# Kernel optimization log

Hardware: AMD Instinct MI355X
Metric: run time of the kernel (lower is better)

The kernel has to match this reference:

```python
import jax, jax.numpy as jnp
import numpy as np

L, B, D, N_LAYERS = 2048, 32, 1024, 4


def setup_inputs() -> dict:
    key = jax.random.key(0)
    ks = jax.random.split(key, 5)
    # PyTorch Linear default init: U(-1/sqrt(fan_in), 1/sqrt(fan_in))
    bound = 1.0 / np.sqrt(D)
    x = jax.random.normal(ks[0], (L, B, D), dtype=jnp.float32)
    A_log = jnp.log(0.99) * jnp.ones((D,), dtype=jnp.float32)  # matches torch init
    layers_W = jax.random.uniform(ks[1], (N_LAYERS, D, D), jnp.float32, -bound, bound)
    layers_b = jax.random.uniform(ks[2], (N_LAYERS, D), jnp.float32, -bound, bound)
    head_W = jax.random.uniform(ks[3], (1, D), jnp.float32, -bound, bound)
    head_b = jax.random.uniform(ks[4], (1,), jnp.float32, -bound, bound)
    return {"x": x, "A_log": A_log, "layers_W": layers_W, "layers_b": layers_b,
            "head_W": head_W, "head_b": head_b}


def reference(x, A_log, layers_W, layers_b, head_W, head_b):
    Lx, Bx, Dx = x.shape
    # log_P[t] = (t+1) * A_log  (cumsum of the constant log_A along time)
    log_P = jnp.cumsum(jnp.broadcast_to(A_log[None, None, :], (Lx, Bx, Dx)), axis=0)
    P = jnp.exp(log_P)                       # [L, B, D]
    h = P * jnp.cumsum(x / P, axis=0)        # diagonal linear SSM scan
    for i in range(layers_W.shape[0]):
        h = jnp.tanh(jnp.einsum('lbd,ed->lbe', h, layers_W[i]) + layers_b[i])
    out = jnp.einsum('lbd,ed->lbe', h, head_W) + head_b  # [L, B, 1]
    return out.squeeze(-1)                   # [L, B]
```

## Files before the change

kernel.cpp:

```cpp
#include <hip/hip_runtime.h>
#include <cstdint>
#include <cstddef>

#define LSEQ 2048
#define BB   32
#define DD   1024
#define NLAYERS 4
#define MM   (LSEQ*BB)
#define BD   (BB*DD)
#define CHUNK 32
#define NCHUNK (LSEQ/CHUNK)

typedef _Float16 f16;
typedef __attribute__((ext_vector_type(8))) _Float16 f16x8;
typedef __attribute__((ext_vector_type(4))) float f32x4;


__global__ void scan_pass1(const float* __restrict__ x, const float* __restrict__ Alog,
                           f16* __restrict__ h, float* __restrict__ carry) {
    int tid = blockIdx.x * blockDim.x + threadIdx.x;
    int bd  = tid & (BD - 1);
    int c   = tid >> 15;
    float a = expf(Alog[bd & (DD - 1)]);
    size_t base = (size_t)c * CHUNK * BD + bd;
    float hv = 0.f;
#pragma unroll
    for (int i = 0; i < CHUNK; ++i) {
        hv = a * hv + x[base + (size_t)i * BD];
        h[base + (size_t)i * BD] = (f16)hv;
    }
    carry[c * BD + bd] = hv;
}

__global__ void scan_pass2(const float* __restrict__ Alog, float* __restrict__ carry) {
    int bd = blockIdx.x * blockDim.x + threadIdx.x;
    float d32 = expf((float)CHUNK * Alog[bd & (DD - 1)]);
    float cin = 0.f;
    for (int c = 0; c < NCHUNK; ++c) {
        float co = carry[c * BD + bd];
        carry[c * BD + bd] = cin;
        cin = d32 * cin + co;
    }
}

__global__ void scan_pass3(const float* __restrict__ Alog, const float* __restrict__ carry,
                           f16* __restrict__ h) {
    int tid = blockIdx.x * blockDim.x + threadIdx.x;
    int bd  = tid & (BD - 1);
    int c   = tid >> 15;
    float a   = expf(Alog[bd & (DD - 1)]);
    float cin = carry[c * BD + bd];
    size_t base = (size_t)c * CHUNK * BD + bd;
    float p = a;
#pragma unroll
    for (int i = 0; i < CHUNK; ++i) {
        size_t idx = base + (size_t)i * BD;
        float hv = (float)h[idx] + p * cin;
        h[idx] = (f16)hv;
        p *= a;
    }
}


__global__ void cvt_w(const float* __restrict__ w, f16* __restrict__ o, int n) {
    int i = (blockIdx.x * blockDim.x + threadIdx.x) * 4;
    if (i + 3 < n) {
        float4 v = *(const float4*)&w[i];
        o[i + 0] = (f16)v.x; o[i + 1] = (f16)v.y;
        o[i + 2] = (f16)v.z; o[i + 3] = (f16)v.w;
    }
}


#define BM 256
#define BN 256
#define BK 64
#define KK 1024
#define NN 1024
#define NKTILE (KK / BK)

__device__ __forceinline__ void gload_lds16(const void* g, void* l) {
    __builtin_amdgcn_global_load_lds((const __attribute__((address_space(1))) unsigned int*)g,
                                     (__attribute__((address_space(3))) unsigned int*)l,
                                     16, 0, 0);
}

__device__ __forceinline__ void stage_half(const f16* __restrict__ gbase, f16* region, int tid) {
#pragma unroll
    for (int j = 0; j < 2; ++j) {
        int s = tid + j * 512;
        int r = s >> 3;
        int c = (s & 7) ^ (r & 7);
        gload_lds16(gbase + (size_t)r * KK + c * 8, region + (size_t)s * 8);
    }
}

__device__ __forceinline__ void stage_tile(const f16* __restrict__ gA, const f16* __restrict__ gW,
                                           f16* As, f16* Bs, int tid) {
    stage_half(gA,                    As,        tid);
    stage_half(gA + (size_t)128 * KK, As + 8192, tid);
    stage_half(gW,                    Bs,        tid);
    stage_half(gW + (size_t)128 * KK, Bs + 8192, tid);
}

__device__ __forceinline__ f16x8 rd(const f16* base, int row, int chunk) {
    int c = chunk ^ (row & 7);
    return *(const f16x8*)(base + row * 64 + c * 8);
}

__device__ __forceinline__ void read12(const f16* Abase, const f16* Bbase,
                                       int arow, int brow, int kc,
                                       f16x8 a[8], f16x8 b[4]) {
#pragma unroll
    for (int m = 0; m < 8; ++m) a[m] = rd(Abase, arow + m * 16, kc);
#pragma unroll
    for (int n = 0; n < 4; ++n) b[n] = rd(Bbase, brow + n * 16, kc);
}

__device__ __forceinline__ float tanh_fast(float z) {
    float e = __expf(2.f * z);
    return 1.f - 2.f / (e + 1.f);
}

#define BAR() do { __builtin_amdgcn_sched_barrier(0); __builtin_amdgcn_s_barrier(); \
                   __builtin_amdgcn_sched_barrier(0); } while (0)

#define MFMA32(av, bv) do {                                                     \
    __builtin_amdgcn_s_setprio(1);                                              \
    _Pragma("unroll")                                                           \
    for (int m = 0; m < 8; ++m)                                                 \
        _Pragma("unroll")                                                       \
        for (int n = 0; n < 4; ++n)                                             \
            acc[m][n] = __builtin_amdgcn_mfma_f32_16x16x32_f16(av[m], bv[n],    \
                                                               acc[m][n], 0, 0, 0); \
    __builtin_amdgcn_s_setprio(0);                                              \
} while (0)

__global__ __launch_bounds__(512, 2) void gemm_tanh(const f16* __restrict__ A,
                                                    const f16* __restrict__ W,
                                                    const float* __restrict__ bias,
                                                    f16* __restrict__ C) {
    __shared__ f16 As[2][BM * BK];
    __shared__ f16 Bs[2][BN * BK];

    const int tid  = threadIdx.x;
    const int lane = tid & 63;
    const int wid  = tid >> 6;
    const int wr   = wid >> 2;
    const int wc   = wid & 3;

    const int cpx = gridDim.x >> 3;
    const int lin = ((int)blockIdx.x & 7) * cpx + ((int)blockIdx.x >> 3);
    const int tm  = (lin >> 2) * BM;
    const int tn  = (lin & 3) * BN;

    const f16* Ab = A + (size_t)tm * KK;
    const f16* Wb = W + (size_t)tn * KK;

    const int fr = lane & 15;
    const int fc = lane >> 4;

    f32x4 acc[8][4];
#pragma unroll
    for (int i = 0; i < 8; ++i)
#pragma unroll
        for (int j = 0; j < 4; ++j)
            acc[i][j] = (f32x4){0.f, 0.f, 0.f, 0.f};

    stage_tile(Ab,      Wb,      &As[0][0], &Bs[0][0], tid);
    stage_tile(Ab + 64, Wb + 64, &As[1][0], &Bs[1][0], tid);
    asm volatile("s_waitcnt vmcnt(8)" ::: "memory");
    BAR();

    const int arow = wr * 128 + fr;
    const int brow = wc * 64  + fr;

    for (int it = 0; it < NKTILE / 2; ++it) {
        const bool pf = (it + 1 < NKTILE / 2);
        f16x8 a0[8], b0[4], a1[8], b1[4];

        read12(&As[0][0], &Bs[0][0], arow, brow, fc,     a0, b0);
        read12(&As[0][0], &Bs[0][0], arow, brow, 4 + fc, a1, b1);
        MFMA32(a0, b0);
        asm volatile("s_waitcnt lgkmcnt(0)" ::: "memory");
        BAR();
        if (pf) stage_tile(Ab + (size_t)(2 * it + 2) * BK, Wb + (size_t)(2 * it + 2) * BK,
                           &As[0][0], &Bs[0][0], tid);
        MFMA32(a1, b1);
        if (pf) asm volatile("s_waitcnt vmcnt(8)" ::: "memory");
        else    asm volatile("s_waitcnt vmcnt(0)" ::: "memory");
        BAR();

        read12(&As[1][0], &Bs[1][0], arow, brow, fc,     a0, b0);
        read12(&As[1][0], &Bs[1][0], arow, brow, 4 + fc, a1, b1);
        MFMA32(a0, b0);
        asm volatile("s_waitcnt lgkmcnt(0)" ::: "memory");
        BAR();
        if (pf) stage_tile(Ab + (size_t)(2 * it + 3) * BK, Wb + (size_t)(2 * it + 3) * BK,
                           &As[1][0], &Bs[1][0], tid);
        MFMA32(a1, b1);
        if (pf) asm volatile("s_waitcnt vmcnt(8)" ::: "memory");
        BAR();
    }

#pragma unroll
    for (int mi = 0; mi < 8; ++mi) {
        const int r0 = tm + wr * 128 + mi * 16 + (fc << 2);
#pragma unroll
        for (int ni = 0; ni < 4; ++ni) {
            const int c = tn + wc * 64 + ni * 16 + fr;
            const float bv = bias[c];
#pragma unroll
            for (int q = 0; q < 4; ++q) {
                float z = acc[mi][ni][q] + bv;
                C[(size_t)(r0 + q) * NN + c] = (f16)tanh_fast(z);
            }
        }
    }
}


__global__ void head_k(const f16* __restrict__ h, const float* __restrict__ hw,
                       const float* __restrict__ hb, float* __restrict__ out) {
    const int row  = blockIdx.x * 4 + (threadIdx.x >> 6);
    const int lane = threadIdx.x & 63;
    const f16* hr = h + (size_t)row * DD;
    float s = 0.f;
#pragma unroll
    for (int j = 0; j < DD / 64; ++j) {
        int d = lane + j * 64;
        s += (float)hr[d] * hw[d];
    }
#pragma unroll
    for (int o = 32; o > 0; o >>= 1) s += __shfl_down(s, o, 64);
    if (lane == 0) out[row] = s + hb[0];
}


extern "C" void kernel_launch(void* const* d_in, const int* in_sizes, int n_in,
                              void* d_out, int out_size, void* d_ws, size_t ws_size,
                              hipStream_t stream) {
    const float* x    = (const float*)d_in[0];
    const float* Alog = (const float*)d_in[1];
    const float* Wls  = (const float*)d_in[2];
    const float* bls  = (const float*)d_in[3];
    const float* hw   = (const float*)d_in[4];
    const float* hb   = (const float*)d_in[5];
    float* out = (float*)d_out;

    char* ws = (char*)d_ws;
    const size_t hbytes = (size_t)MM * DD * sizeof(f16);
    f16* h0 = (f16*)ws;
    f16* h1 = (f16*)(ws + hbytes);
    char* scratch = ws + 2 * hbytes;
    float* carry = (float*)scratch;
    f16*   wf    = (f16*)scratch;

    scan_pass1<<<(NCHUNK * BD) / 256, 256, 0, stream>>>(x, Alog, h0, carry);
    scan_pass2<<<BD / 256, 256, 0, stream>>>(Alog, carry);
    scan_pass3<<<(NCHUNK * BD) / 256, 256, 0, stream>>>(Alog, carry, h0);

    cvt_w<<<(NLAYERS * DD * DD / 4) / 256, 256, 0, stream>>>(Wls, wf, NLAYERS * DD * DD);

    dim3 grid((MM / BM) * (NN / BN)), blk(512);
    gemm_tanh<<<grid, blk, 0, stream>>>(h0, wf + 0 * (DD * DD), bls + 0 * DD, h1);
    gemm_tanh<<<grid, blk, 0, stream>>>(h1, wf + 1 * (DD * DD), bls + 1 * DD, h0);
    gemm_tanh<<<grid, blk, 0, stream>>>(h0, wf + 2 * (DD * DD), bls + 2 * DD, h1);
    gemm_tanh<<<grid, blk, 0, stream>>>(h1, wf + 3 * (DD * DD), bls + 3 * DD, h0);

    head_k<<<MM / 4, 256, 0, stream>>>(h0, hw, hb, out);
}
```

Baseline: 762.7 us.

## Switch GEMM to BK=32 with triple-buffered LDS and one barrier per k-tile

Replaces the double-buffered BK=64 main loop, which used two half-tile MFMA phases and two barriers per tile, with a BK=32 triple-buffered pipeline. Each iteration issues the global->LDS load for tile t+2, reads tile t from LDS, runs one MFMA block, waits on vmcnt and then does a single barrier. The LDS swizzle is reworked for 32-element rows. The aim is to keep more loads in flight and cut barrier overhead per MFMA. In exchange the tiles are smaller, so there are twice as many iterations and barriers overall, with less MFMA work between syncs. LDS use drops from 128KB to 96KB.

New measurement: 837.3 us. 9.8% more time.

```diff
diff --git a/kernel.cpp b/kernel.cpp
--- a/kernel.cpp
+++ b/kernel.cpp
@@ -74,10 +74,10 @@
 
 #define BM 256
 #define BN 256
-#define BK 64
+#define BK 32
 #define KK 1024
 #define NN 1024
-#define NKTILE (KK / BK)
+#define NKT (KK / BK)
 
 __device__ __forceinline__ void gload_lds16(const void* g, void* l) {
     __builtin_amdgcn_global_load_lds((const __attribute__((address_space(1))) unsigned int*)g,
@@ -85,36 +85,27 @@
                                      16, 0, 0);
 }
 
-__device__ __forceinline__ void stage_half(const f16* __restrict__ gbase, f16* region, int tid) {
+__device__ __forceinline__ void stage_kt(const f16* __restrict__ gA, const f16* __restrict__ gW,
+                                         f16* As_, f16* Bs_, int tid) {
 #pragma unroll
     for (int j = 0; j < 2; ++j) {
         int s = tid + j * 512;
-        int r = s >> 3;
-        int c = (s & 7) ^ (r & 7);
-        gload_lds16(gbase + (size_t)r * KK + c * 8, region + (size_t)s * 8);
-    }
-}
-
-__device__ __forceinline__ void stage_tile(const f16* __restrict__ gA, const f16* __restrict__ gW,
-                                           f16* As, f16* Bs, int tid) {
-    stage_half(gA,                    As,        tid);
-    stage_half(gA + (size_t)128 * KK, As + 8192, tid);
-    stage_half(gW,                    Bs,        tid);
-    stage_half(gW + (size_t)128 * KK, Bs + 8192, tid);
+        int r = s >> 2;
+        int c = (s & 3) ^ ((r >> 1) & 3);
+        gload_lds16(gA + (size_t)r * KK + c * 8, As_ + (size_t)s * 8);
+    }
+#pragma unroll
+    for (int j = 0; j < 2; ++j) {
+        int s = tid + j * 512;
+        int r = s >> 2;
+        int c = (s & 3) ^ ((r >> 1) & 3);
+        gload_lds16(gW + (size_t)r * KK + c * 8, Bs_ + (size_t)s * 8);
+    }
 }
 
 __device__ __forceinline__ f16x8 rd(const f16* base, int row, int chunk) {
-    int c = chunk ^ (row & 7);
-    return *(const f16x8*)(base + row * 64 + c * 8);
-}
-
-__device__ __forceinline__ void read12(const f16* Abase, const f16* Bbase,
-                                       int arow, int brow, int kc,
-                                       f16x8 a[8], f16x8 b[4]) {
-#pragma unroll
-    for (int m = 0; m < 8; ++m) a[m] = rd(Abase, arow + m * 16, kc);
-#pragma unroll
-    for (int n = 0; n < 4; ++n) b[n] = rd(Bbase, brow + n * 16, kc);
+    int c = chunk ^ ((row >> 1) & 3);
+    return *(const f16x8*)(base + row * 32 + c * 8);
 }
 
 __device__ __forceinline__ float tanh_fast(float z) {
@@ -124,24 +115,13 @@
 
 #define BAR() do { __builtin_amdgcn_sched_barrier(0); __builtin_amdgcn_s_barrier(); \
                    __builtin_amdgcn_sched_barrier(0); } while (0)
-
-#define MFMA32(av, bv) do {                                                     \
-    __builtin_amdgcn_s_setprio(1);                                              \
-    _Pragma("unroll")                                                           \
-    for (int m = 0; m < 8; ++m)                                                 \
-        _Pragma("unroll")                                                       \
-        for (int n = 0; n < 4; ++n)                                             \
-            acc[m][n] = __builtin_amdgcn_mfma_f32_16x16x32_f16(av[m], bv[n],    \
-                                                               acc[m][n], 0, 0, 0); \
-    __builtin_amdgcn_s_setprio(0);                                              \
-} while (0)
 
 __global__ __launch_bounds__(512, 2) void gemm_tanh(const f16* __restrict__ A,
                                                     const f16* __restrict__ W,
                                                     const float* __restrict__ bias,
                                                     f16* __restrict__ C) {
-    __shared__ f16 As[2][BM * BK];
-    __shared__ f16 Bs[2][BN * BK];
+    __shared__ f16 As[3][BM * BK];
+    __shared__ f16 Bs[3][BN * BK];
 
     const int tid  = threadIdx.x;
     const int lane = tid & 63;
@@ -167,40 +147,39 @@
         for (int j = 0; j < 4; ++j)
             acc[i][j] = (f32x4){0.f, 0.f, 0.f, 0.f};
 
-    stage_tile(Ab,      Wb,      &As[0][0], &Bs[0][0], tid);
-    stage_tile(Ab + 64, Wb + 64, &As[1][0], &Bs[1][0], tid);
-    asm volatile("s_waitcnt vmcnt(8)" ::: "memory");
+    stage_kt(Ab,      Wb,      &As[0][0], &Bs[0][0], tid);
+    stage_kt(Ab + BK, Wb + BK, &As[1][0], &Bs[1][0], tid);
+    asm volatile("s_waitcnt vmcnt(4)" ::: "memory");
     BAR();
 
     const int arow = wr * 128 + fr;
     const int brow = wc * 64  + fr;
 
-    for (int it = 0; it < NKTILE / 2; ++it) {
-        const bool pf = (it + 1 < NKTILE / 2);
-        f16x8 a0[8], b0[4], a1[8], b1[4];
-
-        read12(&As[0][0], &Bs[0][0], arow, brow, fc,     a0, b0);
-        read12(&As[0][0], &Bs[0][0], arow, brow, 4 + fc, a1, b1);
-        MFMA32(a0, b0);
-        asm volatile("s_waitcnt lgkmcnt(0)" ::: "memory");
-        BAR();
-        if (pf) stage_tile(Ab + (size_t)(2 * it + 2) * BK, Wb + (size_t)(2 * it + 2) * BK,
-                           &As[0][0], &Bs[0][0], tid);
-        MFMA32(a1, b1);
-        if (pf) asm volatile("s_waitcnt vmcnt(8)" ::: "memory");
-        else    asm volatile("s_waitcnt vmcnt(0)" ::: "memory");
-        BAR();
-
-        read12(&As[1][0], &Bs[1][0], arow, brow, fc,     a0, b0);
-        read12(&As[1][0], &Bs[1][0], arow, brow, 4 + fc, a1, b1);
-        MFMA32(a0, b0);
-        asm volatile("s_waitcnt lgkmcnt(0)" ::: "memory");
-        BAR();
-        if (pf) stage_tile(Ab + (size_t)(2 * it + 3) * BK, Wb + (size_t)(2 * it + 3) * BK,
-                           &As[1][0], &Bs[1][0], tid);
-        MFMA32(a1, b1);
-        if (pf) asm volatile("s_waitcnt vmcnt(8)" ::: "memory");
-        BAR();
+#pragma unroll
+    for (int t = 0; t < NKT; ++t) {
+        const f16* Ac = &As[t % 3][0];
+        const f16* Bc = &Bs[t % 3][0];
+
+        if (t + 2 < NKT)
+            stage_kt(Ab + (size_t)(t + 2) * BK, Wb + (size_t)(t + 2) * BK,
+                     &As[(t + 2) % 3][0], &Bs[(t + 2) % 3][0], tid);
+
+        f16x8 a[8], b[4];
+#pragma unroll
+        for (int m = 0; m < 8; ++m) a[m] = rd(Ac, arow + m * 16, fc);
+#pragma unroll
+        for (int n = 0; n < 4; ++n) b[n] = rd(Bc, brow + n * 16, fc);
+        __builtin_amdgcn_s_setprio(1);
+#pragma unroll
+        for (int m = 0; m < 8; ++m)
+#pragma unroll
+            for (int n = 0; n < 4; ++n)
+                acc[m][n] = __builtin_amdgcn_mfma_f32_16x16x32_f16(a[m], b[n], acc[m][n], 0, 0, 0);
+        __builtin_amdgcn_s_setprio(0);
+
+        if (t + 2 < NKT)      asm volatile("s_waitcnt vmcnt(4)" ::: "memory");
+        else if (t + 2 == NKT) asm volatile("s_waitcnt vmcnt(0)" ::: "memory");
+        if (t + 1 < NKT) BAR();
     }
 
 #pragma unroll
```
